# Kernel optimization log

Hardware: AMD Instinct MI355X
Metric: run time of the kernel (lower is better)

Reference implementation:

```python
import jax, jax.numpy as jnp
import numpy as np

EMBED_DIM = 768
OUT_DIM = 768
EPS = 1e-06


def setup_inputs() -> dict:
    key = jax.random.key(0)
    ks = jax.random.split(key, 7)
    s_in = 1.0 / np.sqrt(EMBED_DIM)
    x = jax.random.normal(ks[0], (32, 1024, EMBED_DIM), dtype=jnp.float32)
    Wq = jax.random.normal(ks[1], (OUT_DIM, EMBED_DIM), dtype=jnp.float32) * s_in
    bq = jax.random.normal(ks[2], (OUT_DIM,), dtype=jnp.float32) * 0.01
    Wk = jax.random.normal(ks[3], (OUT_DIM, EMBED_DIM), dtype=jnp.float32) * s_in
    bk = jax.random.normal(ks[4], (OUT_DIM,), dtype=jnp.float32) * 0.01
    Wv = jax.random.normal(ks[5], (OUT_DIM, EMBED_DIM), dtype=jnp.float32) * s_in
    bv = jax.random.normal(ks[6], (OUT_DIM,), dtype=jnp.float32) * 0.01
    return {"x": x, "Wq": Wq, "bq": bq, "Wk": Wk, "bk": bk, "Wv": Wv, "bv": bv}


def reference(x, Wq, bq, Wk, bk, Wv, bv):
    # Q/K/V projections: nn.Linear computes x @ W.T + b
    Q = jnp.einsum('bnd,od->bno', x, Wq) + bq  # [B, N, O]
    K = jnp.einsum('bnd,od->bno', x, Wk) + bk
    V = jnp.einsum('bnd,od->bno', x, Wv) + bv
    scale = jnp.sqrt(jnp.asarray(OUT_DIM, dtype=x.dtype)) + EPS
    attn = jnp.einsum('bqo,bko->bqk', Q, K) / scale  # [B, N, N]
    weights = jax.nn.softmax(attn, axis=-1)
    # dropout p=0.0 -> identity (eval/inference)
    return jnp.einsum('bqk,bko->bqo', weights, V)
```

## Files before the change

kernel.cpp:

```cpp
#include <hip/hip_runtime.h>
#include <hip/hip_bf16.h>


typedef float  floatx4  __attribute__((ext_vector_type(4)));
typedef float  floatx16 __attribute__((ext_vector_type(16)));
typedef short  short8   __attribute__((ext_vector_type(8)));

__device__ __forceinline__ unsigned cvtpk(float lo, float hi) {
    unsigned r;
    asm("v_cvt_pk_bf16_f32 %0, %1, %2" : "=v"(r) : "v"(lo), "v"(hi));
    return r;
}
__device__ __forceinline__ floatx16 mfma32(short8 a, short8 b, floatx16 c) {
    return __builtin_amdgcn_mfma_f32_32x32x16_bf16(a, b, c, 0, 0, 0);
}
__device__ __forceinline__ void load_lds16(const void* g, void* lds) {
    __builtin_amdgcn_global_load_lds(
        (const __attribute__((address_space(1))) unsigned int*)g,
        (__attribute__((address_space(3))) unsigned int*)lds, 16, 0, 0);
}
__device__ __forceinline__ void bar_lds() {
    asm volatile("s_waitcnt lgkmcnt(0)" ::: "memory");
    __builtin_amdgcn_s_barrier();
    __builtin_amdgcn_sched_barrier(0);
}

__global__ __launch_bounds__(256) void cvt_bf16(
    const float* __restrict__ s0, unsigned short* __restrict__ d0, int n0,
    const float* __restrict__ s1, unsigned short* __restrict__ d1, int n1,
    const float* __restrict__ s2, unsigned short* __restrict__ d2, int n2)
{
    const int stride = gridDim.x * blockDim.x;
    const int base   = blockIdx.x * blockDim.x + threadIdx.x;
    const float* ss[3] = {s0, s1, s2};
    unsigned short* dd[3] = {d0, d1, d2};
    const int nn[3] = {n0, n1, n2};
#pragma unroll
    for (int j = 0; j < 3; ++j) {
        const floatx4* s = (const floatx4*)ss[j];
        uint4* d = (uint4*)dd[j];
        for (int i = base; i < nn[j]; i += stride) {
            floatx4 v0 = s[2 * i];
            floatx4 v1 = s[2 * i + 1];
            uint4 o;
            o.x = cvtpk(v0[0], v0[1]);
            o.y = cvtpk(v0[2], v0[3]);
            o.z = cvtpk(v1[0], v1[1]);
            o.w = cvtpk(v1[2], v1[3]);
            d[i] = o;
        }
    }
}

__global__ __launch_bounds__(256) void cvt_wfrag(
    const float* __restrict__ W, unsigned short* __restrict__ Wf)
{
    const int i = blockIdx.x * 256 + threadIdx.x;
    const int o  = i / 96;
    const int d0 = (i % 96) * 8;
    const floatx4* s = (const floatx4*)(W + (size_t)o * 768 + d0);
    floatx4 v0 = s[0], v1 = s[1];
    uint4 st;
    st.x = cvtpk(v0[0], v0[1]);
    st.y = cvtpk(v0[2], v0[3]);
    st.z = cvtpk(v1[0], v1[1]);
    st.w = cvtpk(v1[2], v1[3]);
    const size_t idx = (((size_t)(o >> 5) * 48 + (d0 >> 4)) * 64
                        + ((o & 31) | (((d0 >> 3) & 1) << 5))) * 8;
    *reinterpret_cast<uint4*>(Wf + idx) = st;
}

template <int MODE>
__global__ __launch_bounds__(256, 2) void gemm_lds(
    const unsigned short* __restrict__ A,
    const unsigned short* __restrict__ B,
    unsigned short* __restrict__ C, const float* __restrict__ bias,
    float alpha)
{
    __shared__ __align__(16) unsigned short As[2][128 * 64];
    __shared__ __align__(16) unsigned short Bs[2][128 * 64];

    const int tid = threadIdx.x;
    const int l   = tid & 63;
    const int w   = tid >> 6;
    const int wr  = w >> 1;
    const int wc  = w & 1;
    const int lo5 = l & 31;
    const int hi  = l >> 5;
    const int i0  = blockIdx.x * 128;
    const int j0  = blockIdx.y * 128;

    const int srow = l >> 3;
    const int sc16 = (l & 7) ^ srow;
    const unsigned short* Ag = A + (size_t)(i0 + srow) * 768 + sc16 * 8;
    const unsigned short* Bg = B + (size_t)(j0 + srow) * 768 + sc16 * 8;

    floatx16 acc[2][2] = {};

    auto STAGE = [&](int buf, int kt) {
        const int k0 = kt * 64;
#pragma unroll
        for (int t4 = 0; t4 < 4; ++t4) {
            const int t = w * 4 + t4;
            load_lds16(Ag + (size_t)t * 8 * 768 + k0, &As[buf][t * 512]);
            load_lds16(Bg + (size_t)t * 8 * 768 + k0, &Bs[buf][t * 512]);
        }
    };
    auto COMPUTE = [&](int buf) {
        const char* Ab = (const char*)As[buf];
        const char* Bb = (const char*)Bs[buf];
#pragma unroll
        for (int kk = 0; kk < 4; ++kk) {
            short8 a[2], b[2];
#pragma unroll
            for (int i = 0; i < 2; ++i) {
                const int r = wr * 64 + i * 32 + lo5;
                const unsigned off = r * 128 + ((unsigned)((kk * 2 + hi) ^ (r & 7)) << 4);
                a[i] = *reinterpret_cast<const short8*>(Ab + off);
            }
#pragma unroll
            for (int j = 0; j < 2; ++j) {
                const int r = wc * 64 + j * 32 + lo5;
                const unsigned off = r * 128 + ((unsigned)((kk * 2 + hi) ^ (r & 7)) << 4);
                b[j] = *reinterpret_cast<const short8*>(Bb + off);
            }
#pragma unroll
            for (int i = 0; i < 2; ++i)
#pragma unroll
                for (int j = 0; j < 2; ++j)
                    acc[i][j] = mfma32(a[i], b[j], acc[i][j]);
        }
    };

    STAGE(0, 0);
    __syncthreads();
#pragma unroll 1
    for (int kt = 0; kt < 12; ++kt) {
        if (kt + 1 < 12) STAGE((kt + 1) & 1, kt + 1);
        COMPUTE(kt & 1);
        __syncthreads();
    }

#pragma unroll
    for (int i = 0; i < 2; ++i) {
        float bvv[16];
        if (MODE == 0) {
#pragma unroll
            for (int r = 0; r < 16; ++r) {
                const int ol = (r & 3) + 8 * (r >> 2) + 4 * hi;
                bvv[r] = bias[i0 + wr * 64 + i * 32 + ol];
            }
        }
#pragma unroll
        for (int j = 0; j < 2; ++j) {
            float bj = 0.f;
            if (MODE == 1) bj = bias[j0 + wc * 64 + j * 32 + lo5];
            float v[16];
#pragma unroll
            for (int r = 0; r < 16; ++r)
                v[r] = (MODE == 0) ? (acc[i][j][r] + bvv[r]) * alpha
                                   : (acc[i][j][r] + bj);
#pragma unroll
            for (int cc = 0; cc < 2; ++cc) {
                unsigned w0 = cvtpk(v[8 * cc + 0], v[8 * cc + 1]);
                unsigned w1 = cvtpk(v[8 * cc + 2], v[8 * cc + 3]);
                unsigned w2 = cvtpk(v[8 * cc + 4], v[8 * cc + 5]);
                unsigned w3 = cvtpk(v[8 * cc + 6], v[8 * cc + 7]);
                unsigned x0 = __shfl_xor(w0, 32);
                unsigned x1 = __shfl_xor(w1, 32);
                unsigned x2 = __shfl_xor(w2, 32);
                unsigned x3 = __shfl_xor(w3, 32);
                uint4 st;
                st.x = hi ? x2 : w0;
                st.y = hi ? x3 : w1;
                st.z = hi ? w2 : x0;
                st.w = hi ? w3 : x1;
                size_t idx;
                if (MODE == 0) {
                    const int og = i0 + wr * 64 + i * 32 + cc * 16;
                    const int mg = j0 + wc * 64 + j * 32 + lo5;
                    idx = ((size_t)(mg >> 5) * 48 + (og >> 4)) * 512
                        + (size_t)(lo5 | (hi << 5)) * 8;
                } else {
                    const int ng = i0 + wr * 64 + i * 32 + cc * 16;
                    const int dg = j0 + wc * 64 + j * 32 + lo5;
                    idx = ((size_t)(ng >> 4) * 24 + (dg >> 5)) * 512
                        + (size_t)(lo5 | (hi << 5)) * 8;
                }
                *reinterpret_cast<uint4*>(C + idx) = st;
            }
        }
    }
}

__global__ __launch_bounds__(512, 1) void attn_kernel(
    const unsigned short* __restrict__ Wqf,
    const unsigned short* __restrict__ Kf,
    const unsigned short* __restrict__ Vf,
    const float* __restrict__ x,
    const float* __restrict__ bq,
    float* __restrict__ out)
{
    __shared__ __align__(16) unsigned short Q_lds[96 * 512];
    __shared__ __align__(16) unsigned short P_lds[2][32 * 512];

    const int tid = threadIdx.x;
    const int l   = tid & 63;
    const int w   = tid >> 6;
    const int lo5 = l & 31;
    const int hi  = l >> 5;

    const int bid = blockIdx.x;
    const int xcd = bid & 7;
    const int jj  = bid >> 3;
    const int b   = (jj >> 4) * 8 + xcd;
    const int qi  = jj & 15;
    const int q0  = qi * 64;

    const float MFIX  = 12.0f;
    const float alpha = 1.0f / (sqrtf(768.0f) + 1e-6f);

    floatx16 acc6[6] = {};

    {
        float* Xs = (float*)P_lds;
        const float* xg = x + (size_t)(b * 1024 + q0) * 768;
        const short8* Wp = reinterpret_cast<const short8*>(Wqf) + l;

        short8 wbuf[2][3];
#pragma unroll 1
        for (int p = 0; p < 4; ++p) {
#pragma unroll
            for (int it = 0; it < 6; ++it) {
                const int u   = it * 512 + tid;
                const int row = u / 48;
                const int c16 = u % 48;
                load_lds16(xg + (size_t)row * 768 + p * 192 + ((c16 ^ (row & 7)) << 2),
                           &Xs[u * 4]);
            }
            asm volatile("s_waitcnt vmcnt(0)" ::: "memory");
            __builtin_amdgcn_s_barrier();
            __builtin_amdgcn_sched_barrier(0);

            {
                const int ks = p * 12;
#pragma unroll
                for (int jo = 0; jo < 3; ++jo)
                    wbuf[0][jo] = Wp[(size_t)((w * 3 + jo) * 48 + ks) * 64];
            }
#pragma unroll
            for (int it = 0; it < 12; ++it) {
                const int ks = p * 12 + it;
                if (it + 1 < 12) {
#pragma unroll
                    for (int jo = 0; jo < 3; ++jo)
                        wbuf[(it + 1) & 1][jo] =
                            Wp[(size_t)((w * 3 + jo) * 48 + ks + 1) * 64];
                }
                short8 xf[2];
#pragma unroll
                for (int jq = 0; jq < 2; ++jq) {
                    const int row = jq * 32 + lo5;
                    const int un  = it * 4 + hi * 2;
                    floatx4 f0 = *reinterpret_cast<const floatx4*>(
                        &Xs[(row * 48 + ((un + 0) ^ (row & 7))) * 4]);
                    floatx4 f1 = *reinterpret_cast<const floatx4*>(
                        &Xs[(row * 48 + ((un + 1) ^ (row & 7))) * 4]);
                    unsigned q0w = cvtpk(f0[0], f0[1]);
                    unsigned q1w = cvtpk(f0[2], f0[3]);
                    unsigned q2w = cvtpk(f1[0], f1[1]);
                    unsigned q3w = cvtpk(f1[2], f1[3]);
                    uint4 u4 = {q0w, q1w, q2w, q3w};
                    xf[jq] = __builtin_bit_cast(short8, u4);
                }
                __builtin_amdgcn_s_setprio(1);
#pragma unroll
                for (int jo = 0; jo < 3; ++jo) {
#pragma unroll
                    for (int jq = 0; jq < 2; ++jq)
                        acc6[jo * 2 + jq] = mfma32(wbuf[it & 1][jo], xf[jq],
                                                   acc6[jo * 2 + jq]);
                }
                __builtin_amdgcn_s_setprio(0);
            }
            bar_lds();
        }

#pragma unroll
        for (int jo = 0; jo < 3; ++jo) {
            const int o32 = w * 96 + jo * 32;
            float bvv[16];
#pragma unroll
            for (int r = 0; r < 16; ++r)
                bvv[r] = bq[o32 + (r & 3) + 8 * (r >> 2) + 4 * hi];
#pragma unroll
            for (int jq = 0; jq < 2; ++jq) {
                float v[16];
#pragma unroll
                for (int r = 0; r < 16; ++r)
                    v[r] = (acc6[jo * 2 + jq][r] + bvv[r]) * alpha;
#pragma unroll
                for (int cc = 0; cc < 2; ++cc) {
                    unsigned w0 = cvtpk(v[8 * cc + 0], v[8 * cc + 1]);
                    unsigned w1 = cvtpk(v[8 * cc + 2], v[8 * cc + 3]);
                    unsigned w2 = cvtpk(v[8 * cc + 4], v[8 * cc + 5]);
                    unsigned w3 = cvtpk(v[8 * cc + 6], v[8 * cc + 7]);
                    unsigned x0 = __shfl_xor(w0, 32);
                    unsigned x1 = __shfl_xor(w1, 32);
                    unsigned x2 = __shfl_xor(w2, 32);
                    unsigned x3 = __shfl_xor(w3, 32);
                    uint4 st;
                    st.x = hi ? x2 : w0;
                    st.y = hi ? x3 : w1;
                    st.z = hi ? w2 : x0;
                    st.w = hi ? w3 : x1;
                    const int ks_t = w * 6 + jo * 2 + cc;
                    *reinterpret_cast<uint4*>(
                        &Q_lds[((ks_t * 2 + jq) * 64 + (lo5 | (hi << 5))) * 8]) = st;
                }
            }
        }
    }
    bar_lds();

#pragma unroll
    for (int i = 0; i < 6; ++i) acc6[i] = (floatx16){};

    const short8* Kp = reinterpret_cast<const short8*>(Kf)
                       + ((size_t)b * 32 * 48) * 64 + l;
    const short8* Vp = reinterpret_cast<const short8*>(Vf)
                       + ((size_t)b * 64 * 24) * 64 + l;

    float l_reg0 = 0.f, l_reg1 = 0.f;
    short8 kbuf[8], vbuf[4][3];

    {
        const short8* Kc0 = Kp + (size_t)w * 48 * 64;
#pragma unroll
        for (int u = 0; u < 8; ++u) kbuf[u] = Kc0[(size_t)u * 64];
    }

#pragma unroll 1
    for (int c = 0; c < 4; ++c) {
        floatx16 s0 = {}, s1 = {};
        const short8* Kc = Kp + (size_t)(c * 8 + w) * 48 * 64;
        short8 qa0 = *reinterpret_cast<const short8*>(&Q_lds[(0 * 64 + l) * 8]);
        short8 qa1 = *reinterpret_cast<const short8*>(&Q_lds[(1 * 64 + l) * 8]);
#pragma unroll 1
        for (int ks8 = 0; ks8 < 6; ++ks8) {
#pragma unroll
            for (int u = 0; u < 8; ++u) {
                const int ks = ks8 * 8 + u;
                short8 ka = kbuf[u];
                if (ks + 8 < 48) kbuf[u] = Kc[(size_t)(ks + 8) * 64];
                short8 qn0, qn1;
                if (ks + 1 < 48) {
                    qn0 = *reinterpret_cast<const short8*>(&Q_lds[(((ks + 1) * 2 + 0) * 64 + l) * 8]);
                    qn1 = *reinterpret_cast<const short8*>(&Q_lds[(((ks + 1) * 2 + 1) * 64 + l) * 8]);
                }
                __builtin_amdgcn_s_setprio(1);
                s0 = mfma32(ka, qa0, s0);
                s1 = mfma32(ka, qa1, s1);
                __builtin_amdgcn_s_setprio(0);
                qa0 = qn0;
                qa1 = qn1;
            }
        }

        const short8* Vc = Vp + (size_t)(c * 16) * 24 * 64;
#pragma unroll
        for (int g = 0; g < 4; ++g)
#pragma unroll
            for (int jv = 0; jv < 3; ++jv)
                vbuf[g][jv] = Vc[((size_t)g * 24 + w * 3 + jv) * 64];

        if (c < 3) {
            const short8* Kn = Kp + (size_t)((c + 1) * 8 + w) * 48 * 64;
#pragma unroll
            for (int u = 0; u < 8; ++u) kbuf[u] = Kn[(size_t)u * 64];
        }

        float p0[16], p1[16];
        float sum0 = 0.f, sum1 = 0.f;
#pragma unroll
        for (int r = 0; r < 16; ++r) {
            p0[r] = __expf(s0[r] - MFIX); sum0 += p0[r];
            p1[r] = __expf(s1[r] - MFIX); sum1 += p1[r];
        }
        l_reg0 += sum0 + __shfl_xor(sum0, 32);
        l_reg1 += sum1 + __shfl_xor(sum1, 32);

        char* Pb = (char*)P_lds[c & 1];
#pragma unroll
        for (int cc = 0; cc < 2; ++cc) {
#pragma unroll
            for (int jt = 0; jt < 2; ++jt) {
                const float* p = jt ? p1 : p0;
                unsigned w0 = cvtpk(p[8 * cc + 0], p[8 * cc + 1]);
                unsigned w1 = cvtpk(p[8 * cc + 2], p[8 * cc + 3]);
                unsigned w2 = cvtpk(p[8 * cc + 4], p[8 * cc + 5]);
                unsigned w3 = cvtpk(p[8 * cc + 6], p[8 * cc + 7]);
                unsigned x0 = __shfl_xor(w0, 32);
                unsigned x1 = __shfl_xor(w1, 32);
                unsigned x2 = __shfl_xor(w2, 32);
                unsigned x3 = __shfl_xor(w3, 32);
                uint4 st;
                st.x = hi ? x2 : w0;
                st.y = hi ? x3 : w1;
                st.z = hi ? w2 : x0;
                st.w = hi ? w3 : x1;
                const unsigned off = (((unsigned)(w * 2 + cc) * 2 + jt) * 64 + l) * 16;
                *reinterpret_cast<uint4*>(Pb + off) = st;
            }
        }
        bar_lds();

        short8 pa0 = *reinterpret_cast<const short8*>(Pb + ((0 * 64 + l) * 16));
        short8 pa1 = *reinterpret_cast<const short8*>(Pb + ((1 * 64 + l) * 16));
#pragma unroll
        for (int g = 0; g < 16; ++g) {
            short8 pn0, pn1;
            if (g + 1 < 16) {
                pn0 = *reinterpret_cast<const short8*>(Pb + ((((g + 1) * 2 + 0) * 64 + l) * 16));
                pn1 = *reinterpret_cast<const short8*>(Pb + ((((g + 1) * 2 + 1) * 64 + l) * 16));
            }
            short8 v0 = vbuf[g & 3][0];
            short8 v1 = vbuf[g & 3][1];
            short8 v2 = vbuf[g & 3][2];
            if (g < 12) {
#pragma unroll
                for (int jv = 0; jv < 3; ++jv)
                    vbuf[g & 3][jv] = Vc[((size_t)(g + 4) * 24 + w * 3 + jv) * 64];
            }
            __builtin_amdgcn_s_setprio(1);
            acc6[0] = mfma32(pa0, v0, acc6[0]);
            acc6[3] = mfma32(pa1, v0, acc6[3]);
            acc6[1] = mfma32(pa0, v1, acc6[1]);
            acc6[4] = mfma32(pa1, v1, acc6[4]);
            acc6[2] = mfma32(pa0, v2, acc6[2]);
            acc6[5] = mfma32(pa1, v2, acc6[5]);
            __builtin_amdgcn_s_setprio(0);
            pa0 = pn0;
            pa1 = pn1;
        }
    }

    bar_lds();
    float* lred = (float*)Q_lds;
    if (hi == 0) {
        lred[(w * 2 + 0) * 32 + lo5] = l_reg0;
        lred[(w * 2 + 1) * 32 + lo5] = l_reg1;
    }
    bar_lds();
    float lt0 = 0.f, lt1 = 0.f;
#pragma unroll
    for (int wv = 0; wv < 8; ++wv) {
        lt0 += lred[(wv * 2 + 0) * 32 + lo5];
        lt1 += lred[(wv * 2 + 1) * 32 + lo5];
    }
    const float li0 = 1.0f / lt0;
    const float li1 = 1.0f / lt1;

#pragma unroll
    for (int jt = 0; jt < 2; ++jt)
#pragma unroll
        for (int r = 0; r < 16; ++r) {
            const int qr = (r & 3) + 8 * (r >> 2) + 4 * hi;
            const float linv = __shfl(jt ? li1 : li0, qr);
            const size_t grow = (size_t)(b * 1024 + q0 + jt * 32 + qr) * 768;
#pragma unroll
            for (int jv = 0; jv < 3; ++jv)
                out[grow + (w * 3 + jv) * 32 + lo5] = acc6[jt * 3 + jv][r] * linv;
        }
}

extern "C" void kernel_launch(void* const* d_in, const int* in_sizes, int n_in,
                              void* d_out, int out_size, void* d_ws, size_t ws_size,
                              hipStream_t stream) {
    const float* x  = (const float*)d_in[0];
    const float* Wq = (const float*)d_in[1];
    const float* bq = (const float*)d_in[2];
    const float* Wk = (const float*)d_in[3];
    const float* bk = (const float*)d_in[4];
    const float* Wv = (const float*)d_in[5];
    const float* bv = (const float*)d_in[6];
    float* out = (float*)d_out;

    unsigned short* Wqf = (unsigned short*)d_ws;
    unsigned short* Kf  = (unsigned short*)d_ws + 25165824u;
    unsigned short* Vf  = (unsigned short*)d_ws + 50331648u;

    unsigned short* xb  = (unsigned short*)d_out;
    unsigned short* Wkb = (unsigned short*)d_out + 25165824u;
    unsigned short* Wvb = Wkb + 589824u;

    cvt_bf16<<<2048, 256, 0, stream>>>(x, xb, 3145728,
                                       Wk, Wkb, 73728,
                                       Wv, Wvb, 73728);
    cvt_wfrag<<<288, 256, 0, stream>>>(Wq, Wqf);

    gemm_lds<0><<<dim3(6, 256), 256, 0, stream>>>(Wkb, xb, Kf, bk, 1.0f);
    gemm_lds<1><<<dim3(256, 6), 256, 0, stream>>>(xb, Wvb, Vf, bv, 1.0f);

    attn_kernel<<<dim3(512), 512, 0, stream>>>(Wqf, Kf, Vf, x, bq, out);
}
```

Measured before the change: 306.9 us.

## Double-buffer x staging in Q projection and fuse Wq conversion into cvt kernel

The Q-projection prologue of the attention kernel now stages x tiles into two LDS buffers (128 columns per stage, six stages), issuing the next stage's loads before computing on the current one. This overlaps global-to-LDS traffic with MFMA work instead of waiting on each tile. The Wq fragment conversion kernel is merged into the bf16 conversion kernel as extra blocks, saving one launch. The first K-tile prefetch also moves earlier, ahead of the Q epilogue. In exchange, more of P_lds is used for staging and there are more barrier rounds.

```diff
diff --git a/kernel.cpp b/kernel.cpp
--- a/kernel.cpp
+++ b/kernel.cpp
@@ -24,14 +24,36 @@
     __builtin_amdgcn_s_barrier();
     __builtin_amdgcn_sched_barrier(0);
 }
+__device__ __forceinline__ void bar_vm() {
+    asm volatile("s_waitcnt vmcnt(0)" ::: "memory");
+    __builtin_amdgcn_s_barrier();
+    __builtin_amdgcn_sched_barrier(0);
+}
 
 __global__ __launch_bounds__(256) void cvt_bf16(
     const float* __restrict__ s0, unsigned short* __restrict__ d0, int n0,
     const float* __restrict__ s1, unsigned short* __restrict__ d1, int n1,
-    const float* __restrict__ s2, unsigned short* __restrict__ d2, int n2)
+    const float* __restrict__ s2, unsigned short* __restrict__ d2, int n2,
+    const float* __restrict__ W,  unsigned short* __restrict__ Wf)
 {
-    const int stride = gridDim.x * blockDim.x;
-    const int base   = blockIdx.x * blockDim.x + threadIdx.x;
+    if (blockIdx.x >= 2048) {
+        const int i = (blockIdx.x - 2048) * 256 + threadIdx.x;
+        const int o  = i / 96;
+        const int d0i = (i % 96) * 8;
+        const floatx4* s = (const floatx4*)(W + (size_t)o * 768 + d0i);
+        floatx4 v0 = s[0], v1 = s[1];
+        uint4 st;
+        st.x = cvtpk(v0[0], v0[1]);
+        st.y = cvtpk(v0[2], v0[3]);
+        st.z = cvtpk(v1[0], v1[1]);
+        st.w = cvtpk(v1[2], v1[3]);
+        const size_t idx = (((size_t)(o >> 5) * 48 + (d0i >> 4)) * 64
+                            + ((o & 31) | (((d0i >> 3) & 1) << 5))) * 8;
+        *reinterpret_cast<uint4*>(Wf + idx) = st;
+        return;
+    }
+    const int stride = 2048 * 256;
+    const int base   = blockIdx.x * 256 + threadIdx.x;
     const float* ss[3] = {s0, s1, s2};
     unsigned short* dd[3] = {d0, d1, d2};
     const int nn[3] = {n0, n1, n2};
@@ -50,24 +72,6 @@
             d[i] = o;
         }
     }
-}
-
-__global__ __launch_bounds__(256) void cvt_wfrag(
-    const float* __restrict__ W, unsigned short* __restrict__ Wf)
-{
-    const int i = blockIdx.x * 256 + threadIdx.x;
-    const int o  = i / 96;
-    const int d0 = (i % 96) * 8;
-    const floatx4* s = (const floatx4*)(W + (size_t)o * 768 + d0);
-    floatx4 v0 = s[0], v1 = s[1];
-    uint4 st;
-    st.x = cvtpk(v0[0], v0[1]);
-    st.y = cvtpk(v0[2], v0[3]);
-    st.z = cvtpk(v1[0], v1[1]);
-    st.w = cvtpk(v1[2], v1[3]);
-    const size_t idx = (((size_t)(o >> 5) * 48 + (d0 >> 4)) * 64
-                        + ((o & 31) | (((d0 >> 3) & 1) << 5))) * 8;
-    *reinterpret_cast<uint4*>(Wf + idx) = st;
 }
 
 template <int MODE>
@@ -220,41 +224,51 @@
     const float MFIX  = 12.0f;
     const float alpha = 1.0f / (sqrtf(768.0f) + 1e-6f);
 
+    const short8* Kp = reinterpret_cast<const short8*>(Kf)
+                       + ((size_t)b * 32 * 48) * 64 + l;
+    const short8* Vp = reinterpret_cast<const short8*>(Vf)
+                       + ((size_t)b * 64 * 24) * 64 + l;
+
     floatx16 acc6[6] = {};
+    short8 kbuf[8], vbuf[4][3];
 
     {
-        float* Xs = (float*)P_lds;
+        float* Xs0 = (float*)P_lds[0];
+        float* Xs1 = (float*)P_lds[1];
         const float* xg = x + (size_t)(b * 1024 + q0) * 768;
         const short8* Wp = reinterpret_cast<const short8*>(Wqf) + l;
 
-        short8 wbuf[2][3];
+        const int c16 = tid & 31;
+        const int r0  = tid >> 5;
+
+        auto XSTAGE = [&](int p, float* Xs) {
+#pragma unroll
+            for (int it = 0; it < 4; ++it) {
+                const int row = it * 16 + r0;
+                const int u   = it * 512 + tid;
+                load_lds16(xg + (size_t)row * 768 + p * 128 + ((c16 ^ (row & 7)) << 2),
+                           &Xs[u * 4]);
+            }
+        };
+
+        XSTAGE(0, Xs0);
+        bar_vm();
+
+        short8 wbuf2[2][3];
 #pragma unroll 1
-        for (int p = 0; p < 4; ++p) {
-#pragma unroll
-            for (int it = 0; it < 6; ++it) {
-                const int u   = it * 512 + tid;
-                const int row = u / 48;
-                const int c16 = u % 48;
-                load_lds16(xg + (size_t)row * 768 + p * 192 + ((c16 ^ (row & 7)) << 2),
-                           &Xs[u * 4]);
-            }
-            asm volatile("s_waitcnt vmcnt(0)" ::: "memory");
-            __builtin_amdgcn_s_barrier();
-            __builtin_amdgcn_sched_barrier(0);
-
-            {
-                const int ks = p * 12;
-#pragma unroll
-                for (int jo = 0; jo < 3; ++jo)
-                    wbuf[0][jo] = Wp[(size_t)((w * 3 + jo) * 48 + ks) * 64];
-            }
-#pragma unroll
-            for (int it = 0; it < 12; ++it) {
-                const int ks = p * 12 + it;
-                if (it + 1 < 12) {
+        for (int p = 0; p < 6; ++p) {
+            float* Xs = (p & 1) ? Xs1 : Xs0;
+#pragma unroll
+            for (int jo = 0; jo < 3; ++jo)
+                wbuf2[0][jo] = Wp[(size_t)((w * 3 + jo) * 48 + p * 8) * 64];
+            if (p + 1 < 6) XSTAGE(p + 1, (p & 1) ? Xs0 : Xs1);
+#pragma unroll
+            for (int it = 0; it < 8; ++it) {
+                const int ks = p * 8 + it;
+                if (it + 1 < 8) {
 #pragma unroll
                     for (int jo = 0; jo < 3; ++jo)
-                        wbuf[(it + 1) & 1][jo] =
+                        wbuf2[(it + 1) & 1][jo] =
                             Wp[(size_t)((w * 3 + jo) * 48 + ks + 1) * 64];
                 }
                 short8 xf[2];
@@ -263,9 +277,9 @@
                     const int row = jq * 32 + lo5;
                     const int un  = it * 4 + hi * 2;
                     floatx4 f0 = *reinterpret_cast<const floatx4*>(
-                        &Xs[(row * 48 + ((un + 0) ^ (row & 7))) * 4]);
+                        &Xs[((row << 5) + ((un + 0) ^ (row & 7))) * 4]);
                     floatx4 f1 = *reinterpret_cast<const floatx4*>(
-                        &Xs[(row * 48 + ((un + 1) ^ (row & 7))) * 4]);
+                        &Xs[((row << 5) + ((un + 1) ^ (row & 7))) * 4]);
                     unsigned q0w = cvtpk(f0[0], f0[1]);
                     unsigned q1w = cvtpk(f0[2], f0[3]);
                     unsigned q2w = cvtpk(f1[0], f1[1]);
@@ -278,12 +292,18 @@
                 for (int jo = 0; jo < 3; ++jo) {
 #pragma unroll
                     for (int jq = 0; jq < 2; ++jq)
-                        acc6[jo * 2 + jq] = mfma32(wbuf[it & 1][jo], xf[jq],
+                        acc6[jo * 2 + jq] = mfma32(wbuf2[it & 1][jo], xf[jq],
                                                    acc6[jo * 2 + jq]);
                 }
                 __builtin_amdgcn_s_setprio(0);
             }
-            bar_lds();
+            bar_vm();
+        }
+
+        {
+            const short8* Kc0 = Kp + (size_t)w * 48 * 64;
+#pragma unroll
+            for (int u = 0; u < 8; ++u) kbuf[u] = Kc0[(size_t)u * 64];
         }
 
 #pragma unroll
@@ -326,19 +346,7 @@
 #pragma unroll
     for (int i = 0; i < 6; ++i) acc6[i] = (floatx16){};
 
-    const short8* Kp = reinterpret_cast<const short8*>(Kf)
-                       + ((size_t)b * 32 * 48) * 64 + l;
-    const short8* Vp = reinterpret_cast<const short8*>(Vf)
-                       + ((size_t)b * 64 * 24) * 64 + l;
-
     float l_reg0 = 0.f, l_reg1 = 0.f;
-    short8 kbuf[8], vbuf[4][3];
-
-    {
-        const short8* Kc0 = Kp + (size_t)w * 48 * 64;
-#pragma unroll
-        for (int u = 0; u < 8; ++u) kbuf[u] = Kc0[(size_t)u * 64];
-    }
 
 #pragma unroll 1
     for (int c = 0; c < 4; ++c) {
@@ -494,10 +502,10 @@
     unsigned short* Wkb = (unsigned short*)d_out + 25165824u;
     unsigned short* Wvb = Wkb + 589824u;
 
-    cvt_bf16<<<2048, 256, 0, stream>>>(x, xb, 3145728,
+    cvt_bf16<<<2336, 256, 0, stream>>>(x, xb, 3145728,
                                        Wk, Wkb, 73728,
-                                       Wv, Wvb, 73728);
-    cvt_wfrag<<<288, 256, 0, stream>>>(Wq, Wqf);
+                                       Wv, Wvb, 73728,
+                                       Wq, Wqf);
 
     gemm_lds<0><<<dim3(6, 256), 256, 0, stream>>>(Wkb, xb, Kf, bk, 1.0f);
     gemm_lds<1><<<dim3(256, 6), 256, 0, stream>>>(xb, Wvb, Vf, bv, 1.0f);
```

Measured after the change: 306.1 us. About the same (-0.2%).
